# Optimization experiments

Measured on AMD Instinct MI355X. Metric: run time of the kernel, lower is better.

Reference implementation:

```python
import jax, jax.numpy as jnp
import numpy as np

HEADS = 16
HEAD_DIM = 64
HIDDEN = HEADS * HEAD_DIM  # 1024
COMPRESSION = 1.0  # concat([o, p], -1) forces compressed seq len == T, i.e. scale 1
LN_EPS = 1e-5


def _interp_linear_seq(x, scale):
    # F.interpolate(mode='linear', align_corners=False) along the sequence axis.
    # x: [B, T, C] -> [B, int(T*scale), C]
    T = x.shape[1]
    S = int(T * scale)
    src = (jnp.arange(S, dtype=jnp.float32) + 0.5) / scale - 0.5
    src = jnp.clip(src, 0.0, T - 1)
    lo = jnp.floor(src).astype(jnp.int32)
    hi = jnp.minimum(lo + 1, T - 1)
    w = (src - lo.astype(jnp.float32))[None, :, None]
    return x[:, lo] * (1.0 - w) + x[:, hi] * w


def _rotary(x):
    # rotate-half rotary embedding; x: [B, S, h, d]
    S, d = x.shape[1], x.shape[3]
    inv_freq = 1.0 / (10000.0 ** (jnp.arange(0, d, 2, dtype=jnp.float32) / d))
    ang = jnp.arange(S, dtype=jnp.float32)[:, None] * inv_freq  # [S, d/2]
    cos = jnp.cos(ang)[None, :, None, :]
    sin = jnp.sin(ang)[None, :, None, :]
    x1, x2 = jnp.split(x, 2, axis=-1)
    return jnp.concatenate([x1 * cos - x2 * sin, x1 * sin + x2 * cos], axis=-1)


def setup_inputs() -> dict:
    key = jax.random.key(0)
    ks = jax.random.split(key, 4)
    B, T = 4, 2048
    x = jax.random.normal(ks[0], (B, T, HIDDEN), dtype=jnp.float32)
    ln_gamma = jnp.ones((HIDDEN,), dtype=jnp.float32)
    ln_beta = jnp.zeros((HIDDEN,), dtype=jnp.float32)
    w_in = jax.random.normal(ks[1], (HIDDEN, 7 * HIDDEN), dtype=jnp.float32) * (HIDDEN ** -0.5)
    w_out = jax.random.normal(ks[2], (5 * HIDDEN, HIDDEN), dtype=jnp.float32) * ((5 * HIDDEN) ** -0.5)
    b_out = jnp.zeros((HIDDEN,), dtype=jnp.float32)
    return {"x": x, "ln_gamma": ln_gamma, "ln_beta": ln_beta,
            "w_in": w_in, "w_out": w_out, "b_out": b_out}


def reference(x, ln_gamma, ln_beta, w_in, w_out, b_out):
    B, T, _ = x.shape
    # LayerNorm
    mu = jnp.mean(x, axis=-1, keepdims=True)
    var = jnp.mean(jnp.square(x - mu), axis=-1, keepdims=True)
    xn = (x - mu) / jnp.sqrt(var + LN_EPS) * ln_gamma + ln_beta
    # fused QKVP projection (no bias)
    qkvp = xn @ w_in  # [B, T, 7*HIDDEN]
    q, k, v, p = jnp.split(qkvp, [HIDDEN, 2 * HIDDEN, 3 * HIDDEN], axis=-1)
    # linear-interpolation compression of k, v, p along the sequence axis
    k = _interp_linear_seq(k, COMPRESSION)
    v = _interp_linear_seq(v, COMPRESSION)
    p = _interp_linear_seq(p, COMPRESSION)
    S = k.shape[1]
    q = q.reshape(B, T, HEADS, HEAD_DIM)
    k = k.reshape(B, S, HEADS, HEAD_DIM)
    v = v.reshape(B, S, HEADS, HEAD_DIM)
    q = _rotary(q)
    k = _rotary(k)
    # manual softmax attention (no mask in the original)
    a = jnp.einsum('bihd,bjhd->bhij', q, k) * (HEAD_DIM ** -0.5)
    a = jax.nn.softmax(a, axis=-1)
    o = jnp.einsum('bhij,bjhd->bihd', a, v).reshape(B, T, HIDDEN)
    # GELU side branch (torch F.gelu default = exact erf gelu)
    p = jax.nn.gelu(p, approximate=False)
    return jnp.concatenate([o, p], axis=-1) @ w_out + b_out
```

## Files before the change

### kernel.cpp

```cpp
#include <hip/hip_runtime.h>
#include <hip/hip_bf16.h>
#include <math.h>

typedef short bf16x8 __attribute__((ext_vector_type(8)));
typedef float f32x4 __attribute__((ext_vector_type(4)));

#define HEADS 16
#define HDIM 64
#define HID 1024
#define B_ 4
#define T_ 2048
#define BT_ (B_*T_)
#define N1 (7*HID)
#define K2 (5*HID)

#define SM_SCALE_LOG2E 0.18033688011111793f

__device__ __forceinline__ float bf2f(unsigned short u) {
  union { unsigned int i; float f; } c; c.i = ((unsigned int)u) << 16; return c.f;
}
__device__ __forceinline__ unsigned short f2bf(float f) {
  __hip_bfloat16 h = __float2bfloat16(f);
  return __builtin_bit_cast(unsigned short, h);
}
__device__ __forceinline__ unsigned int cvt_pk_bf16(float a, float b) {
  unsigned int r;
  asm("v_cvt_pk_bf16_f32 %0, %1, %2" : "=v"(r) : "v"(a), "v"(b));
  return r;
}
__device__ __forceinline__ float gelu_fast(float x) {
  float y = 0.7978845608028654f * (x + 0.044715f * x * x * x);
  float e = exp2f(y * 2.8853900817779268f);
  float t = 1.f - 2.f / (e + 1.f);
  return 0.5f * x * (1.f + t);
}

__global__ __launch_bounds__(256) void tcast_kernel(const float* __restrict__ in,
                                                    unsigned short* __restrict__ out,
                                                    int R, int C) {
  __shared__ float tile[64][65];
  int tx = threadIdx.x & 63;
  int ty = threadIdx.x >> 6;
  long r0 = (long)blockIdx.y * 64;
  long c0 = (long)blockIdx.x * 64;
#pragma unroll
  for (int i = 0; i < 16; i++) {
    int r = ty + i * 4;
    tile[r][tx] = in[(r0 + r) * C + c0 + tx];
  }
  __syncthreads();
#pragma unroll
  for (int i = 0; i < 16; i++) {
    int rr = ty + i * 4;
    out[(c0 + rr) * R + r0 + tx] = f2bf(tile[tx][rr]);
  }
}

__global__ __launch_bounds__(256) void ln_kernel(const float* __restrict__ x,
                                                 const float* __restrict__ g,
                                                 const float* __restrict__ b,
                                                 unsigned short* __restrict__ xn) {
  int row = blockIdx.x, tid = threadIdx.x;
  float4 v = reinterpret_cast<const float4*>(x + (long)row * HID)[tid];
  float s = v.x + v.y + v.z + v.w;
  float sq = v.x * v.x + v.y * v.y + v.z * v.z + v.w * v.w;
#pragma unroll
  for (int off = 32; off > 0; off >>= 1) { s += __shfl_down(s, off); sq += __shfl_down(sq, off); }
  __shared__ float red[8];
  int wid = tid >> 6, lane = tid & 63;
  if (lane == 0) { red[wid] = s; red[4 + wid] = sq; }
  __syncthreads();
  if (tid == 0) {
    red[0] = red[0] + red[1] + red[2] + red[3];
    red[4] = red[4] + red[5] + red[6] + red[7];
  }
  __syncthreads();
  float mean = red[0] * (1.f / HID);
  float var  = red[4] * (1.f / HID) - mean * mean;
  float rstd = rsqrtf(var + 1e-5f);
  float4 gv = reinterpret_cast<const float4*>(g)[tid];
  float4 bv = reinterpret_cast<const float4*>(b)[tid];
  ushort4 o;
  o.x = f2bf((v.x - mean) * rstd * gv.x + bv.x);
  o.y = f2bf((v.y - mean) * rstd * gv.y + bv.y);
  o.z = f2bf((v.z - mean) * rstd * gv.z + bv.z);
  o.w = f2bf((v.w - mean) * rstd * gv.w + bv.w);
  reinterpret_cast<ushort4*>(xn + (long)row * HID)[tid] = o;
}

__device__ __forceinline__ void gemm_core_db(const unsigned short* __restrict__ A,
                                             const unsigned short* __restrict__ BT,
                                             unsigned short* As, unsigned short* Bs,
                                             int K, int lda, int ldb,
                                             long row0, long col0,
                                             int lane, int wid, f32x4 (&acc)[4][4]) {
  int l15 = lane & 15, lq = lane >> 4;
  int srow = lane >> 2;
  int schnk = lane & 3;
  int r0s = wid * 32 + srow;
  int r1s = r0s + 16;
  int slot0 = schnk ^ ((r0s >> 1) & 3);
  int slot1 = schnk ^ ((r1s >> 1) & 3);
  const unsigned short* a0 = A + (row0 + r0s) * (long)lda + schnk * 8;
  const unsigned short* a1 = A + (row0 + r1s) * (long)lda + schnk * 8;
  const unsigned short* b0 = BT + (col0 + r0s) * (long)ldb + schnk * 8;
  const unsigned short* b1 = BT + (col0 + r1s) * (long)ldb + schnk * 8;
  int wm = (wid & 1) * 64, wn = (wid >> 1) * 64;
  int NT = K / 32;

  bf16x8 ar0 = *reinterpret_cast<const bf16x8*>(a0);
  bf16x8 ar1 = *reinterpret_cast<const bf16x8*>(a1);
  bf16x8 br0 = *reinterpret_cast<const bf16x8*>(b0);
  bf16x8 br1 = *reinterpret_cast<const bf16x8*>(b1);
  *reinterpret_cast<bf16x8*>(&As[r0s * 32 + slot0 * 8]) = ar0;
  *reinterpret_cast<bf16x8*>(&As[r1s * 32 + slot1 * 8]) = ar1;
  *reinterpret_cast<bf16x8*>(&Bs[r0s * 32 + slot0 * 8]) = br0;
  *reinterpret_cast<bf16x8*>(&Bs[r1s * 32 + slot1 * 8]) = br1;
  ar0 = *reinterpret_cast<const bf16x8*>(a0 + 32);
  ar1 = *reinterpret_cast<const bf16x8*>(a1 + 32);
  br0 = *reinterpret_cast<const bf16x8*>(b0 + 32);
  br1 = *reinterpret_cast<const bf16x8*>(b1 + 32);
  __syncthreads();

  int cur = 0;
  for (int t = 0; t < NT; t++) {
    const unsigned short* Asr = As + cur * 4096;
    const unsigned short* Bsr = Bs + cur * 4096;
    bf16x8 af[4], bfv[4];
#pragma unroll
    for (int m = 0; m < 4; m++) {
      int r = wm + m * 16 + l15;
      af[m] = *reinterpret_cast<const bf16x8*>(&Asr[r * 32 + (lq ^ ((r >> 1) & 3)) * 8]);
    }
#pragma unroll
    for (int n = 0; n < 4; n++) {
      int r = wn + n * 16 + l15;
      bfv[n] = *reinterpret_cast<const bf16x8*>(&Bsr[r * 32 + (lq ^ ((r >> 1) & 3)) * 8]);
    }
    if (t + 1 < NT) {
      unsigned short* Asw = As + (cur ^ 1) * 4096;
      unsigned short* Bsw = Bs + (cur ^ 1) * 4096;
      *reinterpret_cast<bf16x8*>(&Asw[r0s * 32 + slot0 * 8]) = ar0;
      *reinterpret_cast<bf16x8*>(&Asw[r1s * 32 + slot1 * 8]) = ar1;
      *reinterpret_cast<bf16x8*>(&Bsw[r0s * 32 + slot0 * 8]) = br0;
      *reinterpret_cast<bf16x8*>(&Bsw[r1s * 32 + slot1 * 8]) = br1;
    }
    if (t + 2 < NT) {
      long ko = (long)(t + 2) * 32;
      ar0 = *reinterpret_cast<const bf16x8*>(a0 + ko);
      ar1 = *reinterpret_cast<const bf16x8*>(a1 + ko);
      br0 = *reinterpret_cast<const bf16x8*>(b0 + ko);
      br1 = *reinterpret_cast<const bf16x8*>(b1 + ko);
    }
#pragma unroll
    for (int m = 0; m < 4; m++)
#pragma unroll
      for (int n = 0; n < 4; n++)
        acc[m][n] = __builtin_amdgcn_mfma_f32_16x16x32_bf16(af[m], bfv[n], acc[m][n], 0, 0, 0);
    __syncthreads();
    cur ^= 1;
  }
}

__global__ __launch_bounds__(256) void gemm1_fused(const unsigned short* __restrict__ A,
                                                   const unsigned short* __restrict__ BT,
                                                   unsigned short* __restrict__ q_r,
                                                   unsigned short* __restrict__ k_r,
                                                   unsigned short* __restrict__ v_t,
                                                   unsigned short* __restrict__ C5) {
  __shared__ unsigned short smem[18432];
  unsigned short* As = smem;
  unsigned short* Bs = smem + 8192;
  int tid = threadIdx.x, lane = tid & 63, wid = tid >> 6;
  long row0 = (long)blockIdx.y * 128;
  long col0 = (long)blockIdx.x * 128;
  f32x4 acc[4][4] = {};
  gemm_core_db(A, BT, As, Bs, HID, HID, HID, row0, col0, lane, wid, acc);

  int wm = (wid & 1) * 64, wn = (wid >> 1) * 64;
  long row_base = row0 + wm;
  int b = (int)(row_base >> 11);
  int t_base = (int)(row_base & 2047);
  int col_base = (int)col0 + wn;
  int region = col_base >> 10;
  int l15 = lane & 15, lq = lane >> 4;

  if (region <= 1) {
    unsigned short* dst = (region == 0) ? q_r : k_r;
    float osc = (region == 0) ? SM_SCALE_LOG2E : 1.0f;
    int head = (col_base & 1023) >> 6;
    long obase = (long)(b * 16 + head) * T_ * 64;
    float fr[2];
    fr[0] = __expf(-(float)l15 * 0.28782313662425572f);
    fr[1] = __expf(-(float)(16 + l15) * 0.28782313662425572f);
#pragma unroll
    for (int m = 0; m < 4; m++) {
#pragma unroll
      for (int j = 0; j < 4; j++) {
        int t = t_base + m * 16 + lq * 4 + j;
#pragma unroll
        for (int n = 0; n < 2; n++) {
          float sn, cs;
          __sincosf((float)t * fr[n], &sn, &cs);
          float xl = acc[m][n][j], xh = acc[m][n + 2][j];
          int d = n * 16 + l15;
          dst[obase + (long)t * 64 + d]      = f2bf((xl * cs - xh * sn) * osc);
          dst[obase + (long)t * 64 + d + 32] = f2bf((xl * sn + xh * cs) * osc);
        }
      }
    }
  } else if (region == 2) {
    int head = (col_base & 1023) >> 6;
    unsigned short* vt = smem + wid * 4608;
#pragma unroll
    for (int m = 0; m < 4; m++)
#pragma unroll
      for (int n = 0; n < 4; n++)
#pragma unroll
        for (int j = 0; j < 4; j++)
          vt[(n * 16 + l15) * 72 + m * 16 + lq * 4 + j] = f2bf(acc[m][n][j]);
    long obase = (long)(b * 16 + head) * 64 * T_;
#pragma unroll
    for (int i = 0; i < 8; i++) {
      int d = i * 8 + (lane >> 3);
      int tl = (lane & 7) * 8;
      bf16x8 v = *reinterpret_cast<const bf16x8*>(&vt[d * 72 + tl]);
      *reinterpret_cast<bf16x8*>(v_t + obase + (long)d * T_ + t_base + tl) = v;
    }
  } else {
    int colp = col_base - 3 * HID;
#pragma unroll
    for (int m = 0; m < 4; m++) {
#pragma unroll
      for (int j = 0; j < 4; j++) {
        long row = row_base + m * 16 + lq * 4 + j;
#pragma unroll
        for (int n = 0; n < 4; n++)
          C5[row * K2 + HID + colp + n * 16 + l15] = f2bf(gelu_fast(acc[m][n][j]));
      }
    }
  }
}

__global__ __launch_bounds__(256) void gemm_bt(const unsigned short* __restrict__ A,
                                               const unsigned short* __restrict__ BT,
                                               float* __restrict__ Cout,
                                               const float* __restrict__ bias,
                                               int K, int lda, int ldb, int ldc) {
  __shared__ unsigned short smem2[16384];
  unsigned short* As = smem2;
  unsigned short* Bs = smem2 + 8192;
  int tid = threadIdx.x, lane = tid & 63, wid = tid >> 6;
  long row0 = (long)blockIdx.y * 128;
  long col0 = (long)blockIdx.x * 128;
  f32x4 acc[4][4] = {};
  gemm_core_db(A, BT, As, Bs, K, lda, ldb, row0, col0, lane, wid, acc);
  int wm = (wid & 1) * 64, wn = (wid >> 1) * 64;
#pragma unroll
  for (int m = 0; m < 4; m++) {
#pragma unroll
    for (int n = 0; n < 4; n++) {
      long r = row0 + wm + m * 16 + (lane >> 4) * 4;
      long c = col0 + wn + n * 16 + (lane & 15);
#pragma unroll
      for (int j = 0; j < 4; j++)
        Cout[(r + j) * (long)ldc + c] = acc[m][n][j] + bias[c];
    }
  }
}

__global__ __launch_bounds__(256) void attn_kernel(const unsigned short* __restrict__ q_r,
                                                   const unsigned short* __restrict__ k_r,
                                                   const unsigned short* __restrict__ v_t,
                                                   unsigned short* __restrict__ C5) {
  int bh = blockIdx.x;
  int qt = blockIdx.y;
  int b = bh >> 4, h = bh & 15;
  int tid = threadIdx.x, lane = tid & 63, wid = tid >> 6;
  int l15 = lane & 15, lq = lane >> 4;
  __shared__ unsigned short Ks[64 * 64];
  __shared__ unsigned short Vts[64 * 64];
  __shared__ unsigned short Ps[4][32 * 64];

  const unsigned short* qbase = q_r + ((long)bh * T_ + qt * 128 + wid * 32) * 64;
  bf16x8 aq[2][2];
#pragma unroll
  for (int m = 0; m < 2; m++)
#pragma unroll
    for (int kk = 0; kk < 2; kk++)
      aq[m][kk] = *reinterpret_cast<const bf16x8*>(
          qbase + (m * 16 + l15) * 64 + kk * 32 + lq * 8);

  f32x4 o_acc[2][4] = {};
  float l_run[2] = {0.f, 0.f};

  const unsigned short* kbase = k_r + (long)bh * T_ * 64;
  const unsigned short* vbase = v_t + (long)bh * 64 * T_;
  int srow = lane >> 3;
  int schnk = lane & 7;
  int slot = schnk ^ srow;
  unsigned short* Pw = &Ps[wid][0];

  bf16x8 kreg[2], vreg[2];
#pragma unroll
  for (int i = 0; i < 2; i++) {
    int c = wid * 2 + i;
    kreg[i] = *reinterpret_cast<const bf16x8*>(kbase + c * 512 + lane * 8);
    vreg[i] = *reinterpret_cast<const bf16x8*>(vbase + (long)(c * 8 + srow) * T_ + schnk * 8);
  }

  for (int kt = 0; kt < 32; kt++) {
#pragma unroll
    for (int i = 0; i < 2; i++) {
      int r = (wid * 2 + i) * 8 + srow;
      *reinterpret_cast<bf16x8*>(&Ks[r * 64 + slot * 8])  = kreg[i];
      *reinterpret_cast<bf16x8*>(&Vts[r * 64 + slot * 8]) = vreg[i];
    }
    if (kt < 31) {
#pragma unroll
      for (int i = 0; i < 2; i++) {
        int c = wid * 2 + i;
        kreg[i] = *reinterpret_cast<const bf16x8*>(kbase + (kt + 1) * 4096 + c * 512 + lane * 8);
        vreg[i] = *reinterpret_cast<const bf16x8*>(vbase + (long)(c * 8 + srow) * T_ + (kt + 1) * 64 + schnk * 8);
      }
    }
    __syncthreads();
    f32x4 s2[4][2] = {};
    __builtin_amdgcn_s_setprio(1);
#pragma unroll
    for (int n = 0; n < 4; n++) {
      int krow = n * 16 + l15;
      bf16x8 kf[2];
#pragma unroll
      for (int kk = 0; kk < 2; kk++)
        kf[kk] = *reinterpret_cast<const bf16x8*>(
            &Ks[krow * 64 + ((kk * 4 + lq) ^ (krow & 7)) * 8]);
#pragma unroll
      for (int m = 0; m < 2; m++)
#pragma unroll
        for (int kk = 0; kk < 2; kk++)
          s2[n][m] = __builtin_amdgcn_mfma_f32_16x16x32_bf16(kf[kk], aq[m][kk], s2[n][m], 0, 0, 0);
    }
    __builtin_amdgcn_s_setprio(0);
#pragma unroll
    for (int m = 0; m < 2; m++) {
      unsigned short* prow = Pw + (m * 16 + l15) * 64;
#pragma unroll
      for (int n = 0; n < 4; n++) {
        float p0 = exp2f(s2[n][m][0]);
        float p1 = exp2f(s2[n][m][1]);
        float p2 = exp2f(s2[n][m][2]);
        float p3 = exp2f(s2[n][m][3]);
        l_run[m] += (p0 + p1) + (p2 + p3);
        unsigned int lo = cvt_pk_bf16(p0, p1);
        unsigned int hi = cvt_pk_bf16(p2, p3);
        int cc = (n * 2 + (lq >> 1)) ^ (l15 & 7);
        uint2 w; w.x = lo; w.y = hi;
        *reinterpret_cast<uint2*>(prow + cc * 8 + (lq & 1) * 4) = w;
      }
    }
    bf16x8 ap[2][2];
#pragma unroll
    for (int m = 0; m < 2; m++)
#pragma unroll
      for (int kk = 0; kk < 2; kk++) {
        int cr = (kk * 4 + lq) ^ (l15 & 7);
        ap[m][kk] = *reinterpret_cast<const bf16x8*>(&Pw[(m * 16 + l15) * 64 + cr * 8]);
      }
    __builtin_amdgcn_s_setprio(1);
#pragma unroll
    for (int n = 0; n < 4; n++) {
      int vrow = n * 16 + l15;
      bf16x8 bv[2];
#pragma unroll
      for (int kk = 0; kk < 2; kk++)
        bv[kk] = *reinterpret_cast<const bf16x8*>(
            &Vts[vrow * 64 + ((kk * 4 + lq) ^ (vrow & 7)) * 8]);
#pragma unroll
      for (int m = 0; m < 2; m++)
#pragma unroll
        for (int kk = 0; kk < 2; kk++)
          o_acc[m][n] = __builtin_amdgcn_mfma_f32_16x16x32_bf16(ap[m][kk], bv[kk], o_acc[m][n], 0, 0, 0);
    }
    __builtin_amdgcn_s_setprio(0);
    __syncthreads();
  }
#pragma unroll
  for (int m = 0; m < 2; m++) {
    float l = l_run[m];
    l += __shfl_xor(l, 16);
    l += __shfl_xor(l, 32);
    l_run[m] = l;
  }
#pragma unroll
  for (int m = 0; m < 2; m++)
#pragma unroll
    for (int j = 0; j < 4; j++) {
      float lsum = __shfl(l_run[m], lq * 4 + j);
      float inv = 1.0f / lsum;
      int tl = qt * 128 + wid * 32 + m * 16 + lq * 4 + j;
      long row = (long)b * T_ + tl;
#pragma unroll
      for (int n = 0; n < 4; n++) {
        int col = h * 64 + n * 16 + l15;
        C5[row * K2 + col] = f2bf(o_acc[m][n][j] * inv);
      }
    }
}

extern "C" void kernel_launch(void* const* d_in, const int* in_sizes, int n_in,
                              void* d_out, int out_size, void* d_ws, size_t ws_size,
                              hipStream_t stream) {
  const float* x     = (const float*)d_in[0];
  const float* g     = (const float*)d_in[1];
  const float* be    = (const float*)d_in[2];
  const float* w_in  = (const float*)d_in[3];
  const float* w_out = (const float*)d_in[4];
  const float* b_out = (const float*)d_in[5];
  float* out = (float*)d_out;

  char* ws = (char*)d_ws;
  size_t off = 0;
  auto alloc = [&](size_t bytes) {
    void* p = ws + off;
    off += (bytes + 255) & ~(size_t)255;
    return p;
  };
  unsigned short* xn     = (unsigned short*)alloc((size_t)BT_ * HID * 2);
  unsigned short* w_inT  = (unsigned short*)alloc((size_t)N1 * HID * 2);
  unsigned short* w_outT = (unsigned short*)alloc((size_t)HID * K2 * 2);
  unsigned short* q_rb   = (unsigned short*)alloc((size_t)BT_ * HID * 2);
  unsigned short* k_rb   = (unsigned short*)alloc((size_t)BT_ * HID * 2);
  unsigned short* v_tb   = (unsigned short*)alloc((size_t)BT_ * HID * 2);
  unsigned short* C5     = (unsigned short*)alloc((size_t)BT_ * K2 * 2);

  tcast_kernel<<<dim3(N1 / 64, HID / 64), 256, 0, stream>>>(w_in, w_inT, HID, N1);
  tcast_kernel<<<dim3(HID / 64, K2 / 64), 256, 0, stream>>>(w_out, w_outT, K2, HID);
  ln_kernel<<<BT_, 256, 0, stream>>>(x, g, be, xn);
  gemm1_fused<<<dim3(N1 / 128, BT_ / 128), 256, 0, stream>>>(xn, w_inT, q_rb, k_rb, v_tb, C5);
  attn_kernel<<<dim3(64, T_ / 128), 256, 0, stream>>>(q_rb, k_rb, v_tb, C5);
  gemm_bt<<<dim3(HID / 128, BT_ / 128), 256, 0, stream>>>(C5, w_outT, out, b_out,
                                                          K2, K2, K2, HID);
}
```

Baseline: 415.3 us.

## Use 32x32 MFMA in attention with register-resident P and double-buffered K/V

Rewrites the attention inner loop to use 32x32x16 bf16 MFMAs instead of 16x16x32. The S tile is turned into the P operand in registers via v_permlane32_swap, which removes the per-wave LDS round trip for P. K/V shared tiles are double-buffered with loads prefetched two tiles ahead, so one barrier per iteration can overlap staging with compute. The costs are higher register pressure (f32x16 accumulators) and doubled LDS for K/V, and correctness depends on the permlane layout mapping being exact.

```diff
diff --git a/kernel.cpp b/kernel.cpp
--- a/kernel.cpp
+++ b/kernel.cpp
@@ -4,6 +4,7 @@
 
 typedef short bf16x8 __attribute__((ext_vector_type(8)));
 typedef float f32x4 __attribute__((ext_vector_type(4)));
+typedef float f32x16 __attribute__((ext_vector_type(16)));
 
 #define HEADS 16
 #define HDIM 64
@@ -27,6 +28,9 @@
   unsigned int r;
   asm("v_cvt_pk_bf16_f32 %0, %1, %2" : "=v"(r) : "v"(a), "v"(b));
   return r;
+}
+__device__ __forceinline__ void permswap(unsigned int& d, unsigned int& s) {
+  asm volatile("v_permlane32_swap_b32 %0, %1" : "+v"(d), "+v"(s));
 }
 __device__ __forceinline__ float gelu_fast(float x) {
   float y = 0.7978845608028654f * (x + 0.044715f * x * x * x);
@@ -277,29 +281,24 @@
   int qt = blockIdx.y;
   int b = bh >> 4, h = bh & 15;
   int tid = threadIdx.x, lane = tid & 63, wid = tid >> 6;
-  int l15 = lane & 15, lq = lane >> 4;
-  __shared__ unsigned short Ks[64 * 64];
-  __shared__ unsigned short Vts[64 * 64];
-  __shared__ unsigned short Ps[4][32 * 64];
+  int l31 = lane & 31, hi = lane >> 5;
+  __shared__ unsigned short Ks[2][64 * 64];
+  __shared__ unsigned short Vts[2][64 * 64];
 
   const unsigned short* qbase = q_r + ((long)bh * T_ + qt * 128 + wid * 32) * 64;
-  bf16x8 aq[2][2];
-#pragma unroll
-  for (int m = 0; m < 2; m++)
-#pragma unroll
-    for (int kk = 0; kk < 2; kk++)
-      aq[m][kk] = *reinterpret_cast<const bf16x8*>(
-          qbase + (m * 16 + l15) * 64 + kk * 32 + lq * 8);
-
-  f32x4 o_acc[2][4] = {};
-  float l_run[2] = {0.f, 0.f};
+  bf16x8 qf[4];
+#pragma unroll
+  for (int kk = 0; kk < 4; kk++)
+    qf[kk] = *reinterpret_cast<const bf16x8*>(qbase + l31 * 64 + kk * 16 + hi * 8);
+
+  f32x16 o_acc[2] = {};
+  float l_run = 0.f;
 
   const unsigned short* kbase = k_r + (long)bh * T_ * 64;
   const unsigned short* vbase = v_t + (long)bh * 64 * T_;
   int srow = lane >> 3;
   int schnk = lane & 7;
   int slot = schnk ^ srow;
-  unsigned short* Pw = &Ps[wid][0];
 
   bf16x8 kreg[2], vreg[2];
 #pragma unroll
@@ -308,104 +307,105 @@
     kreg[i] = *reinterpret_cast<const bf16x8*>(kbase + c * 512 + lane * 8);
     vreg[i] = *reinterpret_cast<const bf16x8*>(vbase + (long)(c * 8 + srow) * T_ + schnk * 8);
   }
-
+#pragma unroll
+  for (int i = 0; i < 2; i++) {
+    int r = (wid * 2 + i) * 8 + srow;
+    *reinterpret_cast<bf16x8*>(&Ks[0][r * 64 + slot * 8])  = kreg[i];
+    *reinterpret_cast<bf16x8*>(&Vts[0][r * 64 + slot * 8]) = vreg[i];
+  }
+#pragma unroll
+  for (int i = 0; i < 2; i++) {
+    int c = wid * 2 + i;
+    kreg[i] = *reinterpret_cast<const bf16x8*>(kbase + 4096 + c * 512 + lane * 8);
+    vreg[i] = *reinterpret_cast<const bf16x8*>(vbase + (long)(c * 8 + srow) * T_ + 64 + schnk * 8);
+  }
+  __syncthreads();
+
+  int cur = 0;
   for (int kt = 0; kt < 32; kt++) {
-#pragma unroll
-    for (int i = 0; i < 2; i++) {
-      int r = (wid * 2 + i) * 8 + srow;
-      *reinterpret_cast<bf16x8*>(&Ks[r * 64 + slot * 8])  = kreg[i];
-      *reinterpret_cast<bf16x8*>(&Vts[r * 64 + slot * 8]) = vreg[i];
-    }
     if (kt < 31) {
+#pragma unroll
+      for (int i = 0; i < 2; i++) {
+        int r = (wid * 2 + i) * 8 + srow;
+        *reinterpret_cast<bf16x8*>(&Ks[cur ^ 1][r * 64 + slot * 8])  = kreg[i];
+        *reinterpret_cast<bf16x8*>(&Vts[cur ^ 1][r * 64 + slot * 8]) = vreg[i];
+      }
+    }
+    if (kt < 30) {
 #pragma unroll
       for (int i = 0; i < 2; i++) {
         int c = wid * 2 + i;
-        kreg[i] = *reinterpret_cast<const bf16x8*>(kbase + (kt + 1) * 4096 + c * 512 + lane * 8);
-        vreg[i] = *reinterpret_cast<const bf16x8*>(vbase + (long)(c * 8 + srow) * T_ + (kt + 1) * 64 + schnk * 8);
-      }
-    }
-    __syncthreads();
-    f32x4 s2[4][2] = {};
+        kreg[i] = *reinterpret_cast<const bf16x8*>(kbase + (kt + 2) * 4096 + c * 512 + lane * 8);
+        vreg[i] = *reinterpret_cast<const bf16x8*>(vbase + (long)(c * 8 + srow) * T_ + (kt + 2) * 64 + schnk * 8);
+      }
+    }
+    const unsigned short* Kc = Ks[cur];
+    const unsigned short* Vc = Vts[cur];
+
+    bf16x8 pa[4];
+#pragma unroll
+    for (int t2 = 0; t2 < 2; t2++) {
+      f32x16 s2 = {};
+      int krow = t2 * 32 + l31;
+      __builtin_amdgcn_s_setprio(1);
+#pragma unroll
+      for (int kk = 0; kk < 4; kk++) {
+        int c = kk * 2 + hi;
+        bf16x8 kf = *reinterpret_cast<const bf16x8*>(&Kc[krow * 64 + (c ^ (krow & 7)) * 8]);
+        s2 = __builtin_amdgcn_mfma_f32_32x32x16_bf16(kf, qf[kk], s2, 0, 0, 0);
+      }
+      __builtin_amdgcn_s_setprio(0);
+      float p[16];
+#pragma unroll
+      for (int r = 0; r < 16; r++) p[r] = exp2f(s2[r]);
+#pragma unroll
+      for (int r = 0; r < 16; r++) l_run += p[r];
+      unsigned int g0 = cvt_pk_bf16(p[0],  p[1]);
+      unsigned int g1 = cvt_pk_bf16(p[2],  p[3]);
+      unsigned int g2 = cvt_pk_bf16(p[4],  p[5]);
+      unsigned int g3 = cvt_pk_bf16(p[6],  p[7]);
+      unsigned int g4 = cvt_pk_bf16(p[8],  p[9]);
+      unsigned int g5 = cvt_pk_bf16(p[10], p[11]);
+      unsigned int g6 = cvt_pk_bf16(p[12], p[13]);
+      unsigned int g7 = cvt_pk_bf16(p[14], p[15]);
+      permswap(g0, g2);
+      permswap(g1, g3);
+      permswap(g4, g6);
+      permswap(g5, g7);
+      uint4 u0; u0.x = g0; u0.y = g1; u0.z = g2; u0.w = g3;
+      uint4 u1; u1.x = g4; u1.y = g5; u1.z = g6; u1.w = g7;
+      pa[t2 * 2]     = __builtin_bit_cast(bf16x8, u0);
+      pa[t2 * 2 + 1] = __builtin_bit_cast(bf16x8, u1);
+    }
     __builtin_amdgcn_s_setprio(1);
 #pragma unroll
-    for (int n = 0; n < 4; n++) {
-      int krow = n * 16 + l15;
-      bf16x8 kf[2];
-#pragma unroll
-      for (int kk = 0; kk < 2; kk++)
-        kf[kk] = *reinterpret_cast<const bf16x8*>(
-            &Ks[krow * 64 + ((kk * 4 + lq) ^ (krow & 7)) * 8]);
-#pragma unroll
-      for (int m = 0; m < 2; m++)
-#pragma unroll
-        for (int kk = 0; kk < 2; kk++)
-          s2[n][m] = __builtin_amdgcn_mfma_f32_16x16x32_bf16(kf[kk], aq[m][kk], s2[n][m], 0, 0, 0);
-    }
-    __builtin_amdgcn_s_setprio(0);
-#pragma unroll
-    for (int m = 0; m < 2; m++) {
-      unsigned short* prow = Pw + (m * 16 + l15) * 64;
-#pragma unroll
-      for (int n = 0; n < 4; n++) {
-        float p0 = exp2f(s2[n][m][0]);
-        float p1 = exp2f(s2[n][m][1]);
-        float p2 = exp2f(s2[n][m][2]);
-        float p3 = exp2f(s2[n][m][3]);
-        l_run[m] += (p0 + p1) + (p2 + p3);
-        unsigned int lo = cvt_pk_bf16(p0, p1);
-        unsigned int hi = cvt_pk_bf16(p2, p3);
-        int cc = (n * 2 + (lq >> 1)) ^ (l15 & 7);
-        uint2 w; w.x = lo; w.y = hi;
-        *reinterpret_cast<uint2*>(prow + cc * 8 + (lq & 1) * 4) = w;
-      }
-    }
-    bf16x8 ap[2][2];
-#pragma unroll
-    for (int m = 0; m < 2; m++)
-#pragma unroll
-      for (int kk = 0; kk < 2; kk++) {
-        int cr = (kk * 4 + lq) ^ (l15 & 7);
-        ap[m][kk] = *reinterpret_cast<const bf16x8*>(&Pw[(m * 16 + l15) * 64 + cr * 8]);
-      }
-    __builtin_amdgcn_s_setprio(1);
-#pragma unroll
-    for (int n = 0; n < 4; n++) {
-      int vrow = n * 16 + l15;
-      bf16x8 bv[2];
-#pragma unroll
-      for (int kk = 0; kk < 2; kk++)
-        bv[kk] = *reinterpret_cast<const bf16x8*>(
-            &Vts[vrow * 64 + ((kk * 4 + lq) ^ (vrow & 7)) * 8]);
-#pragma unroll
-      for (int m = 0; m < 2; m++)
-#pragma unroll
-        for (int kk = 0; kk < 2; kk++)
-          o_acc[m][n] = __builtin_amdgcn_mfma_f32_16x16x32_bf16(ap[m][kk], bv[kk], o_acc[m][n], 0, 0, 0);
+    for (int dt = 0; dt < 2; dt++) {
+      int vrow = dt * 32 + l31;
+#pragma unroll
+      for (int kc = 0; kc < 4; kc++) {
+        int c = kc * 2 + hi;
+        bf16x8 vf = *reinterpret_cast<const bf16x8*>(&Vc[vrow * 64 + (c ^ (vrow & 7)) * 8]);
+        o_acc[dt] = __builtin_amdgcn_mfma_f32_32x32x16_bf16(pa[kc], vf, o_acc[dt], 0, 0, 0);
+      }
     }
     __builtin_amdgcn_s_setprio(0);
     __syncthreads();
-  }
-#pragma unroll
-  for (int m = 0; m < 2; m++) {
-    float l = l_run[m];
-    l += __shfl_xor(l, 16);
-    l += __shfl_xor(l, 32);
-    l_run[m] = l;
-  }
-#pragma unroll
-  for (int m = 0; m < 2; m++)
-#pragma unroll
-    for (int j = 0; j < 4; j++) {
-      float lsum = __shfl(l_run[m], lq * 4 + j);
-      float inv = 1.0f / lsum;
-      int tl = qt * 128 + wid * 32 + m * 16 + lq * 4 + j;
-      long row = (long)b * T_ + tl;
-#pragma unroll
-      for (int n = 0; n < 4; n++) {
-        int col = h * 64 + n * 16 + l15;
-        C5[row * K2 + col] = f2bf(o_acc[m][n][j] * inv);
-      }
-    }
+    cur ^= 1;
+  }
+  float l = l_run;
+  l += __shfl_xor(l, 32);
+#pragma unroll
+  for (int r = 0; r < 16; r++) {
+    int qr = (r & 3) + 8 * (r >> 2) + 4 * hi;
+    float inv = 1.0f / __shfl(l, qr);
+    int tl = qt * 128 + wid * 32 + qr;
+    long row = (long)b * T_ + tl;
+#pragma unroll
+    for (int dt = 0; dt < 2; dt++) {
+      int col = h * 64 + dt * 32 + l31;
+      C5[row * K2 + col] = f2bf(o_acc[dt][r] * inv);
+    }
+  }
 }
 
 extern "C" void kernel_launch(void* const* d_in, const int* in_sizes, int n_in,
```

New measurement: 413.0 us (median of 2 runs). No clear change (-0.5%).
